# Kernel tuning notes

Measured on AMD Instinct MI355X. Metric: run time of the kernel, lower is better.

## Reference

```python
import jax, jax.numpy as jnp
import numpy as np

N_NODES = 10000
N_EDGES = 320000
N_GRAPHS = 64


def _seg_max0(data, seg, num_segments):
    # segment max; empty segments get 0 (matches PyG scatter-max fill behavior)
    agg = jax.ops.segment_max(data, seg, num_segments=num_segments)
    return jnp.where(jnp.isneginf(agg), 0.0, agg)


def _edge_conv(x, src, dst, W, b, n_nodes):
    # PyG EdgeConv: message = nn(cat([x_i, x_j - x_i])), aggr='max' at target i
    xi = x[dst]                       # [E, d]
    xj = x[src]                       # [E, d]
    m = jax.nn.sigmoid(jnp.concatenate([xi, xj - xi], axis=-1) @ W + b)  # [E, d_out]
    return _seg_max0(m, dst, n_nodes)


def setup_inputs() -> dict:
    key = jax.random.key(0)
    ks = jax.random.split(key, 12)
    x = jax.random.normal(ks[0], (N_NODES, 3), dtype=jnp.float32)
    edge_index = jax.random.randint(ks[1], (2, N_EDGES), 0, N_NODES, dtype=jnp.int64)
    batch = jnp.sort(jax.random.randint(ks[2], (N_NODES,), 0, N_GRAPHS, dtype=jnp.int64))

    def lin(k, fan_in, fan_out):
        kw, kb = jax.random.split(k)
        lim = 1.0 / np.sqrt(fan_in)
        W = jax.random.uniform(kw, (fan_in, fan_out), jnp.float32, -lim, lim)
        b = jax.random.uniform(kb, (fan_out,), jnp.float32, -lim, lim)
        return W, b

    W1, b1 = lin(ks[3], 6, 128)     # EdgeConv1 MLP: Linear(2*3, 128)
    W2, b2 = lin(ks[4], 256, 256)   # EdgeConv2 MLP: Linear(2*128, 256)
    W3, b3 = lin(ks[5], 256, 128)   # output Linear(256, 128)
    W4, b4 = lin(ks[6], 128, 10)    # output Linear(128, output_classes)
    return {"x": x, "edge_index": edge_index, "batch": batch,
            "W1": W1, "b1": b1, "W2": W2, "b2": b2,
            "W3": W3, "b3": b3, "W4": W4, "b4": b4}


def reference(x, edge_index, batch, W1, b1, W2, b2, W3, b3, W4, b4):
    src, dst = edge_index[0], edge_index[1]
    h = _edge_conv(x, src, dst, W1, b1, N_NODES)    # [N, 128]
    h = _edge_conv(h, src, dst, W2, b2, N_NODES)    # [N, 256]
    g = _seg_max0(h, batch, N_GRAPHS)               # [G, 256] graph max-pool
    out = jax.nn.sigmoid(g @ W3 + b3) @ W4 + b4     # [G, 10]
    return out
```

## Files before the change

### kernel.cpp

```cpp
#include <hip/hip_runtime.h>

#define N_NODES  10000
#define N_EDGES  320000
#define N_GRAPHS 64
#define STRIDE   192

#define RB 1250
#define RQ 157
#define RW 256

typedef __attribute__((ext_vector_type(8))) __bf16 bf16x8;
typedef __attribute__((ext_vector_type(4))) float f32x4;
typedef __attribute__((ext_vector_type(4))) unsigned int u32x4;

__device__ __forceinline__ float sigm(float z) { return 1.0f / (1.0f + __expf(-z)); }

__device__ __forceinline__ unsigned short f2bf(float f) {
    unsigned int u = __float_as_uint(f);
    return (unsigned short)((u + 0x7fffu + ((u >> 16) & 1u)) >> 16);
}
__device__ __forceinline__ float bf2f(unsigned short h) { return __uint_as_float(((unsigned int)h) << 16); }
__device__ __forceinline__ float bflo(unsigned int u) { return __uint_as_float(u << 16); }
__device__ __forceinline__ float bfhi(unsigned int u) { return __uint_as_float(u & 0xffff0000u); }

__global__ __launch_bounds__(256) void prep_k(
        const unsigned int* __restrict__ ei_raw, const unsigned int* __restrict__ b_raw,
        const float* __restrict__ x, const float* __restrict__ W1,
        const float* __restrict__ W2,
        int* __restrict__ bat, int* __restrict__ cnt, unsigned short* __restrict__ csr_pad,
        unsigned short* __restrict__ Q1,
        unsigned short* __restrict__ Bh, unsigned short* __restrict__ Bl,
        float* __restrict__ g) {
    int bx = blockIdx.x, t = threadIdx.x;
    if (bx < RB) {
        __shared__ int snz[2];
        if (t < 2) snz[t] = 0;
        __syncthreads();
        {
            unsigned int wv = ei_raw[bx * 512 + 2 * t + 1];
            unsigned long long m = __ballot(wv != 0);
            if ((t & 63) == 0 && m) atomicAdd(&snz[0], __popcll(m));
        }
        if (bx * 256 < N_NODES) {
            int w0 = min(bx * 512, N_NODES - 512);
            unsigned int bv = b_raw[w0 + 2 * t + 1];
            unsigned long long m = __ballot(bv != 0);
            if ((t & 63) == 0 && m) atomicAdd(&snz[1], __popcll(m));
        }
        __syncthreads();
        int i = bx * 256 + t;
        int i32e = snz[0] > 16;
        const int* ei = (const int*)ei_raw;
        if (i < N_EDGES) {
            int s = i32e ? ei[i] : ei[2 * i];
            int d = i32e ? ei[N_EDGES + i] : ei[2 * (N_EDGES + i)];
            int slot = atomicAdd(&cnt[d], 1);
            if (slot < STRIDE) csr_pad[d * STRIDE + slot] = (unsigned short)s;
        }
        if (i < N_NODES) {
            int i32b = snz[1] > 16;
            const int* bb = (const int*)b_raw;
            bat[i] = i32b ? bb[i] : bb[2 * i];
        }
    } else if (bx < RB + RQ) {
        __shared__ float xs[192];
        int c = t & 127, half = t >> 7;
        float k0 = W1[384 + c];
        float k1 = W1[512 + c];
        float k2 = W1[640 + c];
        int n0 = (bx - RB) * 64;
        int nmax = min(64, N_NODES - n0);
        if (t < 192) xs[t] = (t < nmax * 3) ? x[n0 * 3 + t] : 0.f;
        __syncthreads();
        for (int tt = 0; tt < 32; tt++) {
            int ln = 2 * tt + half;
            if (ln < nmax) {
                float v = xs[ln * 3 + 0] * k0 + xs[ln * 3 + 1] * k1 + xs[ln * 3 + 2] * k2;
                Q1[(n0 + ln) * 128 + c] = f2bf(v);
            }
        }
    } else if (bx < RB + RQ + RW) {
        int idx = (bx - RB - RQ) * 256 + t;
        int nn = idx >> 7, k = idx & 127;
        float wc;
        if (nn < 256) wc = W2[k * 256 + nn] - W2[(128 + k) * 256 + nn];
        else          wc = W2[(128 + k) * 256 + (nn - 256)];
        unsigned short h = f2bf(wc);
        Bh[idx] = h;
        Bl[idx] = f2bf(wc - bf2f(h));
    } else {
        float4 z = make_float4(0.f, 0.f, 0.f, 0.f);
#pragma unroll
        for (int it = 0; it < 16; it++) *(float4*)&g[(t + it * 256) * 4] = z;
    }
}

__global__ __launch_bounds__(256) void econv1_k(
        const float* __restrict__ x, const float* __restrict__ W1, const float* __restrict__ b1,
        const unsigned int* __restrict__ Q1u,
        const int* __restrict__ cnt, const unsigned short* __restrict__ csr_pad,
        unsigned short* __restrict__ h1h, unsigned short* __restrict__ h1l) {
    int lane = threadIdx.x & 63;
    int i = blockIdx.x * 4 + (threadIdx.x >> 6);
    if (i >= N_NODES) return;
    int e = min(cnt[i], STRIDE);
    float o0 = 0.f, o1 = 0.f;
    if (e > 0) {
        const unsigned short* row = csr_pad + (size_t)i * STRIDE;
        float z0 = -3.4e38f, z1 = -3.4e38f;
        int last = e - 1;
        for (int k = 0; k < e; k += 16) {
            uint4 ra = *(const uint4*)&row[k];
            uint4 rb = *(const uint4*)&row[k + 8];
            unsigned int rw[8] = {ra.x, ra.y, ra.z, ra.w, rb.x, rb.y, rb.z, rb.w};
            int j0 = rw[0] & 0xffff;
            unsigned int u[16];
#pragma unroll
            for (int tt = 0; tt < 16; tt++) {
                int raw = (rw[tt >> 1] >> ((tt & 1) * 16)) & 0xffff;
                int j = (k + tt <= last) ? raw : j0;
                u[tt] = Q1u[j * 64 + lane];
            }
#pragma unroll
            for (int tt = 0; tt < 16; tt++) {
                z0 = fmaxf(z0, bflo(u[tt]));
                z1 = fmaxf(z1, bfhi(u[tt]));
            }
        }
        float x0 = x[i * 3 + 0], x1 = x[i * 3 + 1], x2 = x[i * 3 + 2];
        int c0 = 2 * lane, c1 = 2 * lane + 1;
        float p0 = b1[c0] + x0 * (W1[c0] - W1[384 + c0]) + x1 * (W1[128 + c0] - W1[512 + c0]) +
                   x2 * (W1[256 + c0] - W1[640 + c0]);
        float p1 = b1[c1] + x0 * (W1[c1] - W1[384 + c1]) + x1 * (W1[128 + c1] - W1[512 + c1]) +
                   x2 * (W1[256 + c1] - W1[640 + c1]);
        o0 = sigm(p0 + z0);
        o1 = sigm(p1 + z1);
    }
    unsigned short hh0 = f2bf(o0), hh1 = f2bf(o1);
    unsigned short hl0 = f2bf(o0 - bf2f(hh0)), hl1 = f2bf(o1 - bf2f(hh1));
    *(ushort2*)&h1h[i * 128 + 2 * lane] = make_ushort2(hh0, hh1);
    *(ushort2*)&h1l[i * 128 + 2 * lane] = make_ushort2(hl0, hl1);
}

__global__ __launch_bounds__(256) void gemm2_k(
        const unsigned short* __restrict__ Ahg, const unsigned short* __restrict__ Alg,
        const unsigned short* __restrict__ Bhg, const unsigned short* __restrict__ Blg,
        const float* __restrict__ b2, float* __restrict__ P2,
        unsigned short* __restrict__ Q2, int n) {
    __shared__ __align__(16) char smem[65536];
    char* Ahb = smem;
    char* Alb = smem + 16384;
    char* Bhb = smem + 32768;
    char* Blb = smem + 49152;
    int t = threadIdx.x;
    int m0 = blockIdx.x * 64;
    int n0 = blockIdx.y * 64;
#pragma unroll
    for (int it = 0; it < 4; it++) {
        int c = t + it * 256;
        int row = c >> 4, kb = c & 15;
        int dsa = (row * 256 + kb * 16) ^ ((row & 7) << 4);
        u32x4 va = {0u, 0u, 0u, 0u}, vl = {0u, 0u, 0u, 0u};
        if (m0 + row < n) {
            va = *(const u32x4*)&Ahg[(m0 + row) * 128 + kb * 8];
            vl = *(const u32x4*)&Alg[(m0 + row) * 128 + kb * 8];
        }
        *(u32x4*)(Ahb + dsa) = va;
        *(u32x4*)(Alb + dsa) = vl;
        *(u32x4*)(Bhb + dsa) = *(const u32x4*)&Bhg[(n0 + row) * 128 + kb * 8];
        *(u32x4*)(Blb + dsa) = *(const u32x4*)&Blg[(n0 + row) * 128 + kb * 8];
    }
    __syncthreads();

    int w = t >> 6, lane = t & 63;
    int lr = lane & 15, lg = lane >> 4;
    int am = 16 * w + lr;
    int abase = am * 256 + lg * 16;
    int asw = (am & 7) << 4;
    bf16x8 ah[4], al[4];
#pragma unroll
    for (int kk = 0; kk < 4; kk++) {
        int off = (abase + kk * 64) ^ asw;
        ah[kk] = *(const bf16x8*)(Ahb + off);
        al[kk] = *(const bf16x8*)(Alb + off);
    }
    int bsw = (lr & 7) << 4;
#pragma unroll
    for (int nt = 0; nt < 4; nt++) {
        int nb = (nt * 16 + lr) * 256 + lg * 16;
        f32x4 acc = {0.f, 0.f, 0.f, 0.f};
#pragma unroll
        for (int kk = 0; kk < 4; kk++) {
            int off = (nb + kk * 64) ^ bsw;
            bf16x8 bh = *(const bf16x8*)(Bhb + off);
            bf16x8 bl = *(const bf16x8*)(Blb + off);
            acc = __builtin_amdgcn_mfma_f32_16x16x32_bf16(ah[kk], bh, acc, 0, 0, 0);
            acc = __builtin_amdgcn_mfma_f32_16x16x32_bf16(al[kk], bh, acc, 0, 0, 0);
            acc = __builtin_amdgcn_mfma_f32_16x16x32_bf16(ah[kk], bl, acc, 0, 0, 0);
        }
        int colg = n0 + nt * 16 + lr;
        int mbase = m0 + 16 * w + 4 * lg;
        if (colg < 256) {
            float bias = b2[colg];
#pragma unroll
            for (int r = 0; r < 4; r++) {
                int m = mbase + r;
                if (m < n)
                    __builtin_nontemporal_store(acc[r] + bias, &P2[(size_t)m * 256 + colg]);
            }
        } else {
            int qc = colg - 256;
#pragma unroll
            for (int r = 0; r < 4; r++) {
                int m = mbase + r;
                if (m < n) Q2[(size_t)m * 256 + qc] = f2bf(acc[r]);
            }
        }
    }
}

__global__ __launch_bounds__(256) void econv2_k(
        const float* __restrict__ P2, const unsigned int* __restrict__ Q2u,
        const int* __restrict__ cnt, const unsigned short* __restrict__ csr_pad,
        const int* __restrict__ bat, float* __restrict__ g) {
    int lane = threadIdx.x & 63;
    int w = threadIdx.x >> 6;
    int i = blockIdx.x * 2 + (w >> 1);
    if (i >= N_NODES) return;
    int e = min(cnt[i], STRIDE);
    if (e == 0) return;
    int cc = (w & 1) * 64 + lane;
    const unsigned short* row = csr_pad + (size_t)i * STRIDE;
    float z0 = -3.4e38f, z1 = -3.4e38f;
    int last = e - 1;
    for (int k = 0; k < e; k += 16) {
        uint4 ra = *(const uint4*)&row[k];
        uint4 rb = *(const uint4*)&row[k + 8];
        unsigned int rw[8] = {ra.x, ra.y, ra.z, ra.w, rb.x, rb.y, rb.z, rb.w};
        int j0 = rw[0] & 0xffff;
        unsigned int u[16];
#pragma unroll
        for (int tt = 0; tt < 16; tt++) {
            int raw = (rw[tt >> 1] >> ((tt & 1) * 16)) & 0xffff;
            int j = (k + tt <= last) ? raw : j0;
            u[tt] = Q2u[j * 128 + cc];
        }
#pragma unroll
        for (int tt = 0; tt < 16; tt++) {
            z0 = fmaxf(z0, bflo(u[tt]));
            z1 = fmaxf(z1, bfhi(u[tt]));
        }
    }
    unsigned long long pv =
        __builtin_nontemporal_load((const unsigned long long*)&P2[(size_t)i * 256 + 2 * cc]);
    float px = __uint_as_float((unsigned int)pv);
    float py = __uint_as_float((unsigned int)(pv >> 32));
    int gb = bat[i] * 256 + 2 * cc;
    atomicMax((unsigned int*)&g[gb + 0], __float_as_uint(sigm(px + z0)));
    atomicMax((unsigned int*)&g[gb + 1], __float_as_uint(sigm(py + z1)));
}

__global__ void final_k(const float* __restrict__ g, const float* __restrict__ W3,
                        const float* __restrict__ b3, const float* __restrict__ W4,
                        const float* __restrict__ b4, float* __restrict__ out) {
    __shared__ float gs[256];
    __shared__ float ss[128];
    int b = blockIdx.x, t = threadIdx.x;
    gs[t] = g[b * 256 + t];
    gs[t + 128] = g[b * 256 + 128 + t];
    __syncthreads();
    float acc = b3[t];
#pragma unroll 8
    for (int k = 0; k < 256; k++) acc += gs[k] * W3[k * 128 + t];
    ss[t] = sigm(acc);
    __syncthreads();
    if (t < 10) {
        float o = b4[t];
#pragma unroll 8
        for (int k = 0; k < 128; k++) o += ss[k] * W4[k * 10 + t];
        out[b * 10 + t] = o;
    }
}

extern "C" void kernel_launch(void* const* d_in, const int* in_sizes, int n_in,
                              void* d_out, int out_size, void* d_ws, size_t ws_size,
                              hipStream_t stream) {
    const float* x  = (const float*)d_in[0];
    const void*  ei_raw = d_in[1];
    const void*  b_raw  = d_in[2];
    const float* W1 = (const float*)d_in[3];
    const float* b1 = (const float*)d_in[4];
    const float* W2 = (const float*)d_in[5];
    const float* b2 = (const float*)d_in[6];
    const float* W3 = (const float*)d_in[7];
    const float* b3 = (const float*)d_in[8];
    const float* W4 = (const float*)d_in[9];
    const float* b4 = (const float*)d_in[10];

    char* ws = (char*)d_ws;
    size_t off = 0;
    auto alloc = [&](size_t bytes) {
        void* p = ws + off;
        off += (bytes + 255) & ~(size_t)255;
        return p;
    };
    int*            bat     = (int*)alloc(N_NODES * 4);
    int*            cnt     = (int*)alloc(N_NODES * 4);
    unsigned short* csr_pad = (unsigned short*)alloc((size_t)N_NODES * STRIDE * 2);
    unsigned short* Q1      = (unsigned short*)alloc((size_t)N_NODES * 128 * 2);
    unsigned short* h1h     = (unsigned short*)alloc((size_t)N_NODES * 128 * 2);
    unsigned short* h1l     = (unsigned short*)alloc((size_t)N_NODES * 128 * 2);
    unsigned short* Bh      = (unsigned short*)alloc(512 * 128 * 2);
    unsigned short* Bl      = (unsigned short*)alloc(512 * 128 * 2);
    float*          P2      = (float*)alloc((size_t)N_NODES * 256 * 4);
    unsigned short* Q2      = (unsigned short*)alloc((size_t)N_NODES * 256 * 2);
    float*          g       = (float*)alloc(N_GRAPHS * 256 * 4);

    hipMemsetAsync(cnt, 0, N_NODES * 4, stream);

    prep_k<<<RB + RQ + RW + 1, 256, 0, stream>>>(
        (const unsigned int*)ei_raw, (const unsigned int*)b_raw, x, W1, W2,
        bat, cnt, csr_pad, Q1, Bh, Bl, g);

    econv1_k<<<(N_NODES + 3) / 4, 256, 0, stream>>>(x, W1, b1, (const unsigned int*)Q1,
                                                    cnt, csr_pad, h1h, h1l);
    gemm2_k<<<dim3((N_NODES + 63) / 64, 8), 256, 0, stream>>>(h1h, h1l, Bh, Bl, b2, P2, Q2, N_NODES);

    econv2_k<<<(N_NODES + 1) / 2, 256, 0, stream>>>(P2, (const unsigned int*)Q2,
                                                    cnt, csr_pad, bat, g);
    final_k<<<N_GRAPHS, 128, 0, stream>>>(g, W3, b3, W4, b4, (float*)d_out);
}
```

Baseline: 179.2 us.

## Split neighbor-max gathers across two waves per node and widen edge loads

Both EdgeConv aggregation kernels now split each node's neighbor list between two wavefronts that take alternating 16-edge chunks. The partial maxima are combined through shared memory after a barrier, so each node gets twice the memory-level parallelism for its irregular gathers. The prep kernel now handles two edges per thread with vectorized index loads, which halves its edge-block count. The cost is doubled blocks for econv2, a block-wide sync, and an idle second wave during the epilogue.

```diff
diff --git a/kernel.cpp b/kernel.cpp
--- a/kernel.cpp
+++ b/kernel.cpp
@@ -5,7 +5,7 @@
 #define N_GRAPHS 64
 #define STRIDE   192
 
-#define RB 1250
+#define RB 625
 #define RQ 157
 #define RW 256
 
@@ -37,7 +37,7 @@
         if (t < 2) snz[t] = 0;
         __syncthreads();
         {
-            unsigned int wv = ei_raw[bx * 512 + 2 * t + 1];
+            unsigned int wv = ei_raw[bx * 1024 + 2 * t + 1];
             unsigned long long m = __ballot(wv != 0);
             if ((t & 63) == 0 && m) atomicAdd(&snz[0], __popcll(m));
         }
@@ -48,15 +48,24 @@
             if ((t & 63) == 0 && m) atomicAdd(&snz[1], __popcll(m));
         }
         __syncthreads();
-        int i = bx * 256 + t;
         int i32e = snz[0] > 16;
         const int* ei = (const int*)ei_raw;
-        if (i < N_EDGES) {
-            int s = i32e ? ei[i] : ei[2 * i];
-            int d = i32e ? ei[N_EDGES + i] : ei[2 * (N_EDGES + i)];
-            int slot = atomicAdd(&cnt[d], 1);
-            if (slot < STRIDE) csr_pad[d * STRIDE + slot] = (unsigned short)s;
-        }
+        int e0 = bx * 512 + 2 * t;
+        int s0, s1, d0, d1;
+        if (i32e) {
+            uint2 sv = *(const uint2*)&ei[e0];
+            uint2 dv = *(const uint2*)&ei[N_EDGES + e0];
+            s0 = sv.x; s1 = sv.y; d0 = dv.x; d1 = dv.y;
+        } else {
+            uint4 sv = *(const uint4*)&ei[2 * e0];
+            uint4 dv = *(const uint4*)&ei[2 * (N_EDGES + e0)];
+            s0 = sv.x; s1 = sv.z; d0 = dv.x; d1 = dv.z;
+        }
+        int slot = atomicAdd(&cnt[d0], 1);
+        if (slot < STRIDE) csr_pad[d0 * STRIDE + slot] = (unsigned short)s0;
+        slot = atomicAdd(&cnt[d1], 1);
+        if (slot < STRIDE) csr_pad[d1 * STRIDE + slot] = (unsigned short)s1;
+        int i = bx * 256 + t;
         if (i < N_NODES) {
             int i32b = snz[1] > 16;
             const int* bb = (const int*)b_raw;
@@ -100,25 +109,28 @@
         const unsigned int* __restrict__ Q1u,
         const int* __restrict__ cnt, const unsigned short* __restrict__ csr_pad,
         unsigned short* __restrict__ h1h, unsigned short* __restrict__ h1l) {
+    __shared__ float2 zsh[2][2][64];
     int lane = threadIdx.x & 63;
-    int i = blockIdx.x * 4 + (threadIdx.x >> 6);
-    if (i >= N_NODES) return;
+    int w = threadIdx.x >> 6;
+    int nb = w >> 1, par = w & 1;
+    int i = blockIdx.x * 2 + nb;
     int e = min(cnt[i], STRIDE);
-    float o0 = 0.f, o1 = 0.f;
+    float z0 = -3.4e38f, z1 = -3.4e38f;
     if (e > 0) {
         const unsigned short* row = csr_pad + (size_t)i * STRIDE;
-        float z0 = -3.4e38f, z1 = -3.4e38f;
         int last = e - 1;
-        for (int k = 0; k < e; k += 16) {
-            uint4 ra = *(const uint4*)&row[k];
-            uint4 rb = *(const uint4*)&row[k + 8];
+        int nchunks = (e + 15) >> 4;
+        for (int c = par; c < nchunks; c += 2) {
+            int k0 = c << 4;
+            uint4 ra = *(const uint4*)&row[k0];
+            uint4 rb = *(const uint4*)&row[k0 + 8];
             unsigned int rw[8] = {ra.x, ra.y, ra.z, ra.w, rb.x, rb.y, rb.z, rb.w};
             int j0 = rw[0] & 0xffff;
             unsigned int u[16];
 #pragma unroll
             for (int tt = 0; tt < 16; tt++) {
                 int raw = (rw[tt >> 1] >> ((tt & 1) * 16)) & 0xffff;
-                int j = (k + tt <= last) ? raw : j0;
+                int j = (k0 + tt <= last) ? raw : j0;
                 u[tt] = Q1u[j * 64 + lane];
             }
 #pragma unroll
@@ -127,19 +139,29 @@
                 z1 = fmaxf(z1, bfhi(u[tt]));
             }
         }
-        float x0 = x[i * 3 + 0], x1 = x[i * 3 + 1], x2 = x[i * 3 + 2];
-        int c0 = 2 * lane, c1 = 2 * lane + 1;
-        float p0 = b1[c0] + x0 * (W1[c0] - W1[384 + c0]) + x1 * (W1[128 + c0] - W1[512 + c0]) +
-                   x2 * (W1[256 + c0] - W1[640 + c0]);
-        float p1 = b1[c1] + x0 * (W1[c1] - W1[384 + c1]) + x1 * (W1[128 + c1] - W1[512 + c1]) +
-                   x2 * (W1[256 + c1] - W1[640 + c1]);
-        o0 = sigm(p0 + z0);
-        o1 = sigm(p1 + z1);
-    }
-    unsigned short hh0 = f2bf(o0), hh1 = f2bf(o1);
-    unsigned short hl0 = f2bf(o0 - bf2f(hh0)), hl1 = f2bf(o1 - bf2f(hh1));
-    *(ushort2*)&h1h[i * 128 + 2 * lane] = make_ushort2(hh0, hh1);
-    *(ushort2*)&h1l[i * 128 + 2 * lane] = make_ushort2(hl0, hl1);
+    }
+    zsh[nb][par][lane] = make_float2(z0, z1);
+    __syncthreads();
+    if (par == 0) {
+        float o0 = 0.f, o1 = 0.f;
+        if (e > 0) {
+            float2 oz = zsh[nb][1][lane];
+            z0 = fmaxf(z0, oz.x);
+            z1 = fmaxf(z1, oz.y);
+            float x0 = x[i * 3 + 0], x1 = x[i * 3 + 1], x2 = x[i * 3 + 2];
+            int c0 = 2 * lane, c1 = 2 * lane + 1;
+            float p0 = b1[c0] + x0 * (W1[c0] - W1[384 + c0]) +
+                       x1 * (W1[128 + c0] - W1[512 + c0]) + x2 * (W1[256 + c0] - W1[640 + c0]);
+            float p1 = b1[c1] + x0 * (W1[c1] - W1[384 + c1]) +
+                       x1 * (W1[128 + c1] - W1[512 + c1]) + x2 * (W1[256 + c1] - W1[640 + c1]);
+            o0 = sigm(p0 + z0);
+            o1 = sigm(p1 + z1);
+        }
+        unsigned short hh0 = f2bf(o0), hh1 = f2bf(o1);
+        unsigned short hl0 = f2bf(o0 - bf2f(hh0)), hl1 = f2bf(o1 - bf2f(hh1));
+        *(ushort2*)&h1h[i * 128 + 2 * lane] = make_ushort2(hh0, hh1);
+        *(ushort2*)&h1l[i * 128 + 2 * lane] = make_ushort2(hl0, hl1);
+    }
 }
 
 __global__ __launch_bounds__(256) void gemm2_k(
@@ -223,26 +245,29 @@
         const float* __restrict__ P2, const unsigned int* __restrict__ Q2u,
         const int* __restrict__ cnt, const unsigned short* __restrict__ csr_pad,
         const int* __restrict__ bat, float* __restrict__ g) {
+    __shared__ float2 zsh[2][2][64];
+    int i = blockIdx.x;
+    int e = min(cnt[i], STRIDE);
+    if (e == 0) return;
     int lane = threadIdx.x & 63;
     int w = threadIdx.x >> 6;
-    int i = blockIdx.x * 2 + (w >> 1);
-    if (i >= N_NODES) return;
-    int e = min(cnt[i], STRIDE);
-    if (e == 0) return;
-    int cc = (w & 1) * 64 + lane;
+    int half = w & 1, par = w >> 1;
+    int cc = half * 64 + lane;
     const unsigned short* row = csr_pad + (size_t)i * STRIDE;
     float z0 = -3.4e38f, z1 = -3.4e38f;
     int last = e - 1;
-    for (int k = 0; k < e; k += 16) {
-        uint4 ra = *(const uint4*)&row[k];
-        uint4 rb = *(const uint4*)&row[k + 8];
+    int nchunks = (e + 15) >> 4;
+    for (int c = par; c < nchunks; c += 2) {
+        int k0 = c << 4;
+        uint4 ra = *(const uint4*)&row[k0];
+        uint4 rb = *(const uint4*)&row[k0 + 8];
         unsigned int rw[8] = {ra.x, ra.y, ra.z, ra.w, rb.x, rb.y, rb.z, rb.w};
         int j0 = rw[0] & 0xffff;
         unsigned int u[16];
 #pragma unroll
         for (int tt = 0; tt < 16; tt++) {
             int raw = (rw[tt >> 1] >> ((tt & 1) * 16)) & 0xffff;
-            int j = (k + tt <= last) ? raw : j0;
+            int j = (k0 + tt <= last) ? raw : j0;
             u[tt] = Q2u[j * 128 + cc];
         }
 #pragma unroll
@@ -251,13 +276,20 @@
             z1 = fmaxf(z1, bfhi(u[tt]));
         }
     }
-    unsigned long long pv =
-        __builtin_nontemporal_load((const unsigned long long*)&P2[(size_t)i * 256 + 2 * cc]);
-    float px = __uint_as_float((unsigned int)pv);
-    float py = __uint_as_float((unsigned int)(pv >> 32));
-    int gb = bat[i] * 256 + 2 * cc;
-    atomicMax((unsigned int*)&g[gb + 0], __float_as_uint(sigm(px + z0)));
-    atomicMax((unsigned int*)&g[gb + 1], __float_as_uint(sigm(py + z1)));
+    zsh[half][par][lane] = make_float2(z0, z1);
+    __syncthreads();
+    if (par == 0) {
+        float2 oz = zsh[half][1][lane];
+        z0 = fmaxf(z0, oz.x);
+        z1 = fmaxf(z1, oz.y);
+        unsigned long long pv =
+            __builtin_nontemporal_load((const unsigned long long*)&P2[(size_t)i * 256 + 2 * cc]);
+        float px = __uint_as_float((unsigned int)pv);
+        float py = __uint_as_float((unsigned int)(pv >> 32));
+        int gb = bat[i] * 256 + 2 * cc;
+        atomicMax((unsigned int*)&g[gb + 0], __float_as_uint(sigm(px + z0)));
+        atomicMax((unsigned int*)&g[gb + 1], __float_as_uint(sigm(py + z1)));
+    }
 }
 
 __global__ void final_k(const float* __restrict__ g, const float* __restrict__ W3,
@@ -322,11 +354,11 @@
         (const unsigned int*)ei_raw, (const unsigned int*)b_raw, x, W1, W2,
         bat, cnt, csr_pad, Q1, Bh, Bl, g);
 
-    econv1_k<<<(N_NODES + 3) / 4, 256, 0, stream>>>(x, W1, b1, (const unsigned int*)Q1,
-                                                    cnt, csr_pad, h1h, h1l);
+    econv1_k<<<N_NODES / 2, 256, 0, stream>>>(x, W1, b1, (const unsigned int*)Q1,
+                                              cnt, csr_pad, h1h, h1l);
     gemm2_k<<<dim3((N_NODES + 63) / 64, 8), 256, 0, stream>>>(h1h, h1l, Bh, Bl, b2, P2, Q2, N_NODES);
 
-    econv2_k<<<(N_NODES + 1) / 2, 256, 0, stream>>>(P2, (const unsigned int*)Q2,
-                                                    cnt, csr_pad, bat, g);
+    econv2_k<<<N_NODES, 256, 0, stream>>>(P2, (const unsigned int*)Q2,
+                                          cnt, csr_pad, bat, g);
     final_k<<<N_GRAPHS, 128, 0, stream>>>(g, W3, b3, W4, b4, (float*)d_out);
 }
```

Result: no change. 177.5 us (-0.9%).
